# Kernel optimization log

Hardware: AMD Instinct MI355X
Metric: run time of the kernel (lower is better)

## Reference

```python
import jax, jax.numpy as jnp
import numpy as np

EMB = 2048
HEADS = 16
HEAD_DIM = EMB // HEADS
MIN_WINDOW = 64
MAX_WINDOW = 256
ROPE_BASE = 10000.0


def setup_inputs() -> dict:
    key = jax.random.key(0)
    ks = jax.random.split(key, 5)
    B, S = 2, 2048
    x = jax.random.normal(ks[0], (B, S, EMB), dtype=jnp.float32)
    w_qkv = jax.random.normal(ks[1], (3 * EMB, EMB), dtype=jnp.float32) * (EMB ** -0.5)
    w_out = jax.random.normal(ks[2], (EMB, EMB), dtype=jnp.float32) * (EMB ** -0.5)
    w_c1 = jax.random.normal(ks[3], (EMB // 4, EMB), dtype=jnp.float32) * 0.1 * (EMB ** -0.5)
    w_c2 = jax.random.normal(ks[4], (1, EMB // 4), dtype=jnp.float32) * 0.1 * ((EMB // 4) ** -0.5)
    return {"x": x, "w_qkv": w_qkv, "w_out": w_out, "w_c1": w_c1, "w_c2": w_c2}


def _rotate_half(t):
    # interleaved pairs: [-x1, x0, -x3, x2, ...]
    x1 = t[..., ::2]
    x2 = t[..., 1::2]
    return jnp.stack((-x2, x1), axis=-1).reshape(t.shape)


def _rope_tables(seq_len, dtype):
    inv_freq = 1.0 / (ROPE_BASE ** (jnp.arange(0, HEAD_DIM, 2, dtype=jnp.float32) / HEAD_DIM))
    pos = jnp.arange(seq_len, dtype=jnp.float32)
    freqs = jnp.outer(pos, inv_freq)                      # [S, D/2]
    emb = jnp.concatenate([freqs, freqs], axis=-1)        # [S, D]
    return jnp.cos(emb)[None, None].astype(dtype), jnp.sin(emb)[None, None].astype(dtype)


def _forward(x, w_qkv, w_out, w_c1, w_c2):
    B, S, _ = x.shape
    scale = HEAD_DIM ** -0.5

    qkv = x @ w_qkv.T                                     # [B, S, 3E]
    qkv = qkv.reshape(B, S, 3, HEADS, HEAD_DIM).transpose(2, 0, 3, 1, 4)
    q, k, v = qkv[0], qkv[1], qkv[2]                      # each [B, H, S, D]

    cos, sin = _rope_tables(S, x.dtype)
    q = q * cos + _rotate_half(q) * sin
    k = k * cos + _rotate_half(k) * sin

    scores = jnp.einsum("bhqd,bhkd->bhqk", q, k) * scale  # [B, H, S, S]

    # adaptive window size from input complexity
    var = jnp.var(x.reshape(B, -1), axis=1, ddof=1)        # torch unbiased var over dims [1,2]
    var_norm = jax.nn.sigmoid(var * 10.0 - 5.0)
    x_mean = x.mean(axis=1)                                # [B, E]
    hidden = jax.nn.silu(x_mean @ w_c1.T)
    learned = jax.nn.sigmoid(hidden @ w_c2.T)[:, 0]        # [B]
    complexity = (var_norm + learned) / 2.0
    window_f = MIN_WINDOW + complexity * (MAX_WINDOW - MIN_WINDOW)
    window = window_f.mean().astype(jnp.int32)             # trunc like .int()
    window = jnp.maximum(jnp.minimum(window, S), MIN_WINDOW)

    # causal + sliding-window mask: keep 0 <= q_pos - k_pos < window
    pos = jnp.arange(S)
    rel = pos[:, None] - pos[None, :]                      # [S, S]
    keep = (rel >= 0) & (rel < window)
    scores = jnp.where(keep[None, None], scores, -jnp.inf)

    attn = jax.nn.softmax(scores, axis=-1)
    out = jnp.einsum("bhqk,bhkd->bhqd", attn, v)           # [B, H, S, D]
    out = out.transpose(0, 2, 1, 3).reshape(B, S, EMB)
    return out @ w_out.T


def reference(x, w_qkv, w_out, w_c1, w_c2):
    return _forward(x, w_qkv, w_out, w_c1, w_c2)
```

## Files before the change

kernel.cpp:

```cpp
#include <hip/hip_runtime.h>
#include <math.h>


#define S_LEN 2048
#define EMB 2048
#define HEADS 16
#define HDIM 128
#define NT 20
#define PSTR 336

typedef _Float16 f16x8 __attribute__((ext_vector_type(8)));
typedef _Float16 f16x4 __attribute__((ext_vector_type(4)));
typedef float f32x4 __attribute__((ext_vector_type(4)));

__device__ __forceinline__ void gld16(const void* g, void* l) {
    __builtin_amdgcn_global_load_lds(
        (const __attribute__((address_space(1))) unsigned int*)g,
        (__attribute__((address_space(3))) unsigned int*)l, 16, 0, 0);
}

__global__ void rope_table(float2* __restrict__ cstab) {
    int s = blockIdx.x;
    int d = threadIdx.x;
    int j = d & 63;
    double inv = pow(10000.0, -(double)j / 64.0);
    double ang = (double)s * inv;
    cstab[s * HDIM + d] = make_float2((float)cos(ang), (float)sin(ang));
}

__global__ __launch_bounds__(256) void col_reduce(const float* __restrict__ x,
                                                  float* __restrict__ xmean_acc,
                                                  double* __restrict__ scal,
                                                  _Float16* __restrict__ x16) {
    int b = blockIdx.z;
    int cg = blockIdx.x;
    int sg = blockIdx.y;
    int e4 = cg * 256 + threadIdx.x;
    const size_t base = ((size_t)b * S_LEN + sg * 32) * EMB;
    const float4* xb = (const float4*)(x + base) + e4;
    f16x4* xo = (f16x4*)(x16 + base) + e4;
    double cs0 = 0.0, cs1 = 0.0, cs2 = 0.0, cs3 = 0.0;
    double cq = 0.0;
    for (int s = 0; s < 32; ++s) {
        float4 v = xb[(size_t)s * (EMB / 4)];
        f16x4 o;
        o.x = (_Float16)v.x; o.y = (_Float16)v.y;
        o.z = (_Float16)v.z; o.w = (_Float16)v.w;
        xo[(size_t)s * (EMB / 4)] = o;
        cs0 += v.x; cs1 += v.y; cs2 += v.z; cs3 += v.w;
        cq += (double)v.x * v.x + (double)v.y * v.y +
              (double)v.z * v.z + (double)v.w * v.w;
    }
    float* xm = xmean_acc + b * EMB + e4 * 4;
    atomicAdd(xm + 0, (float)cs0);
    atomicAdd(xm + 1, (float)cs1);
    atomicAdd(xm + 2, (float)cs2);
    atomicAdd(xm + 3, (float)cs3);
    __shared__ double rs[256], rq[256];
    rs[threadIdx.x] = cs0 + cs1 + cs2 + cs3;
    rq[threadIdx.x] = cq;
    __syncthreads();
    for (int off = 128; off > 0; off >>= 1) {
        if (threadIdx.x < off) {
            rs[threadIdx.x] += rs[threadIdx.x + off];
            rq[threadIdx.x] += rq[threadIdx.x + off];
        }
        __syncthreads();
    }
    if (threadIdx.x == 0) {
        atomicAdd(&scal[b], rs[0]);
        atomicAdd(&scal[2 + b], rq[0]);
    }
}

__global__ __launch_bounds__(256) void hidden_kernel(const float* __restrict__ xmean_acc,
                                                     const float* __restrict__ wc1,
                                                     float* __restrict__ hidden) {
    int j = blockIdx.x;
    int b = blockIdx.y;
    const float* xm = xmean_acc + b * EMB;
    const float* wr = wc1 + (size_t)j * EMB;
    double acc = 0.0;
    for (int k = threadIdx.x; k < EMB; k += 256)
        acc += (double)xm[k] * (double)wr[k];
    __shared__ double red[256];
    red[threadIdx.x] = acc;
    __syncthreads();
    for (int off = 128; off > 0; off >>= 1) {
        if (threadIdx.x < off) red[threadIdx.x] += red[threadIdx.x + off];
        __syncthreads();
    }
    if (threadIdx.x == 0) {
        double z = red[0] * (1.0 / 2048.0);
        hidden[b * 512 + j] = (float)(z / (1.0 + exp(-z)));
    }
}

__global__ __launch_bounds__(512) void window_kernel(const float* __restrict__ hidden,
                                                     const float* __restrict__ wc2,
                                                     const double* __restrict__ scal,
                                                     int* __restrict__ wout) {
    __shared__ double red[512];
    __shared__ double wfs[2];
    for (int b = 0; b < 2; ++b) {
        red[threadIdx.x] = (double)hidden[b * 512 + threadIdx.x] * (double)wc2[threadIdx.x];
        __syncthreads();
        for (int off = 256; off > 0; off >>= 1) {
            if (threadIdx.x < off) red[threadIdx.x] += red[threadIdx.x + off];
            __syncthreads();
        }
        if (threadIdx.x == 0) {
            double pre = red[0];
            double learned = 1.0 / (1.0 + exp(-pre));
            const double N = (double)S_LEN * (double)EMB;
            double sum = scal[b], sq = scal[2 + b];
            double var = (sq - sum * sum / N) / (N - 1.0);
            double vn = 1.0 / (1.0 + exp(-(var * 10.0 - 5.0)));
            double comp = 0.5 * (vn + learned);
            wfs[b] = 64.0 + comp * 192.0;
        }
        __syncthreads();
    }
    if (threadIdx.x == 0) {
        float wf = (float)(0.5 * (wfs[0] + wfs[1]));
        int w = (int)wf;
        if (w > S_LEN) w = S_LEN;
        if (w < 64) w = 64;
        *wout = w;
    }
}

#define NQKV4 3145728
#define NOUT4 1048576
__global__ __launch_bounds__(256) void cvt_weights(const float* __restrict__ wqkv,
                                                   const float* __restrict__ wout,
                                                   _Float16* __restrict__ d_qkv,
                                                   _Float16* __restrict__ d_out) {
    int i = blockIdx.x * 256 + threadIdx.x;
    const float4* s;
    f16x4* d;
    if (i < NQKV4) {
        s = (const float4*)wqkv + i;
        d = (f16x4*)d_qkv + i;
    } else {
        s = (const float4*)wout + (i - NQKV4);
        d = (f16x4*)d_out + (i - NQKV4);
    }
    float4 v = *s;
    f16x4 o;
    o.x = (_Float16)v.x; o.y = (_Float16)v.y;
    o.z = (_Float16)v.z; o.w = (_Float16)v.w;
    *d = o;
}

#define GEMM_PROLOGUE(An, Wn)                                                   \
    __shared__ _Float16 As[128 * 64];                                           \
    __shared__ _Float16 Bs[128 * 64];                                           \
    const int tid = threadIdx.x;                                                \
    const int lane = tid & 63;                                                  \
    const int wv = tid >> 6;                                                    \
    const int wm = wv >> 1, wn = wv & 1;                                        \
    const int m0 = blockIdx.y * 128;                                            \
    const int n0 = blockIdx.x * 128;                                            \
    const int lrow = lane >> 3;                                       \
    const int lchk = (lane & 7) ^ lrow;                       \
    const int srow = wv * 32 + lrow;                                            \
    const _Float16* agp = An + (size_t)(m0 + srow) * EMB + lchk * 8;            \
    const _Float16* bgp = Wn + (size_t)(n0 + srow) * EMB + lchk * 8;            \
    _Float16* al = &As[wv * 32 * 64];                                           \
    _Float16* bl = &Bs[wv * 32 * 64];                                           \
    const int frow = lane & 15;                                                 \
    const int fgrp = lane >> 4;                                                 \
    f32x4 acc[4][4] = {};                                                       \
    for (int k0 = 0; k0 < EMB; k0 += 64) {                                      \
        __syncthreads();                                                        \
        _Pragma("unroll")                                                       \
        for (int t = 0; t < 4; ++t) {                                           \
            gld16(agp + (size_t)t * 8 * EMB, al + t * 8 * 64);                  \
            gld16(bgp + (size_t)t * 8 * EMB, bl + t * 8 * 64);                  \
        }                                                                       \
        agp += 64; bgp += 64;                                                   \
        __syncthreads();                                                        \
        _Pragma("unroll")                                                       \
        for (int ks = 0; ks < 2; ++ks) {                                        \
            f16x8 af[4], bf[4];                                                 \
            _Pragma("unroll")                                                   \
            for (int i = 0; i < 4; ++i)                                         \
                af[i] = *(const f16x8*)&As[(wm * 64 + i * 16 + frow) * 64 +     \
                                           (((ks * 4 + fgrp) ^ (frow & 7)) * 8)]; \
            _Pragma("unroll")                                                   \
            for (int j = 0; j < 4; ++j)                                         \
                bf[j] = *(const f16x8*)&Bs[(wn * 64 + j * 16 + frow) * 64 +     \
                                           (((ks * 4 + fgrp) ^ (frow & 7)) * 8)]; \
            _Pragma("unroll")                                                   \
            for (int i = 0; i < 4; ++i)                                         \
                _Pragma("unroll")                                               \
                for (int j = 0; j < 4; ++j)                                     \
                    acc[i][j] = __builtin_amdgcn_mfma_f32_16x16x32_f16(         \
                        af[i], bf[j], acc[i][j], 0, 0, 0);                      \
        }                                                                       \
    }                                                                           \
    const int colbase = lane & 15;                                              \
    const int rowoff = (lane >> 4) * 4;

__global__ __launch_bounds__(256) void gemm_qkv_f16(const _Float16* __restrict__ An,
                                                    const _Float16* __restrict__ Wn,
                                                    _Float16* __restrict__ q16,
                                                    _Float16* __restrict__ k16,
                                                    _Float16* __restrict__ vt,
                                                    const float2* __restrict__ cstab) {
    GEMM_PROLOGUE(An, Wn)
    const int which = n0 >> 11;
    const int h = (n0 >> 7) & 15;
    if (which == 2) {
#pragma unroll
        for (int i = 0; i < 4; ++i) {
#pragma unroll
            for (int j = 0; j < 4; ++j) {
                const int d = wn * 64 + j * 16 + colbase;
                int m = m0 + wm * 64 + i * 16 + rowoff;
                int b = m >> 11, s = m & 2047;
                f16x4 o;
#pragma unroll
                for (int r = 0; r < 4; ++r) o[r] = (_Float16)acc[i][j][r];
                *(f16x4*)&vt[(((size_t)b * HEADS + h) * HDIM + d) * S_LEN + s] = o;
            }
        }
    } else {
        _Float16* dst = which == 0 ? q16 : k16;
        const float sgn = (colbase & 1) ? 1.f : -1.f;
#pragma unroll
        for (int i = 0; i < 4; ++i) {
#pragma unroll
            for (int j = 0; j < 4; ++j) {
                const int d = wn * 64 + j * 16 + colbase;
#pragma unroll
                for (int r = 0; r < 4; ++r) {
                    int m = m0 + wm * 64 + i * 16 + rowoff + r;
                    int b = m >> 11, s = m & 2047;
                    float a = acc[i][j][r];
                    float p = __shfl_xor(a, 1, 64);
                    float2 cs = cstab[(size_t)s * HDIM + d];
                    float o = fmaf(a, cs.x, sgn * p * cs.y);
                    dst[(((size_t)b * HEADS + h) * S_LEN + s) * HDIM + d] = (_Float16)o;
                }
            }
        }
    }
}

__global__ __launch_bounds__(256) void gemm_out_f16(const _Float16* __restrict__ An,
                                                    const _Float16* __restrict__ Wn,
                                                    float* __restrict__ C) {
    GEMM_PROLOGUE(An, Wn)
#pragma unroll
    for (int i = 0; i < 4; ++i) {
#pragma unroll
        for (int j = 0; j < 4; ++j) {
            const int n = n0 + wn * 64 + j * 16 + colbase;
#pragma unroll
            for (int r = 0; r < 4; ++r) {
                int m = m0 + wm * 64 + i * 16 + rowoff + r;
                C[(size_t)m * EMB + n] = acc[i][j][r];
            }
        }
    }
}

__global__ __launch_bounds__(256) void attn_mfma(const _Float16* __restrict__ q16,
                                                 const _Float16* __restrict__ k16,
                                                 const _Float16* __restrict__ v16t,
                                                 _Float16* __restrict__ ob,
                                                 const int* __restrict__ wptr) {
    const int q0 = blockIdx.x * 64;
    const int h = blockIdx.y;
    const int b = blockIdx.z;
    const int tid = threadIdx.x;
    const int lane = tid & 63;
    const int wv = tid >> 6;
    const int w = *wptr;

    __shared__ _Float16 Pl[4][16 * PSTR];
    _Float16* Pw = Pl[wv];

    const int kstart = q0 - 256;
    int ntlo_w = (257 - w) >> 4;
    int ntlo_n = q0 < 256 ? ((256 - q0) >> 4) : 0;
    const int ntlo = ntlo_w > ntlo_n ? ntlo_w : ntlo_n;

    const int frow = lane & 15;
    const int fgrp = lane >> 4;
    const int fcol = fgrp * 8;

    const size_t bh = (size_t)b * HEADS + h;
    const _Float16* Qp = q16 + (bh * S_LEN + q0 + wv * 16 + frow) * HDIM + fcol;
    const _Float16* Kb = k16 + bh * S_LEN * HDIM;
    const _Float16* Vt = v16t + bh * HDIM * S_LEN;

    f16x8 aq[4];
#pragma unroll
    for (int ks = 0; ks < 4; ++ks) aq[ks] = *(const f16x8*)(Qp + ks * 32);

    f32x4 accs[NT];
#pragma unroll
    for (int nt = 0; nt < NT; ++nt) accs[nt] = (f32x4){0.f, 0.f, 0.f, 0.f};
#pragma unroll
    for (int nt = 0; nt < NT; ++nt) {
        if (nt < ntlo) continue;
        int krow = kstart + nt * 16 + frow;
        if (krow < 0) krow = 0;
        const _Float16* kp = Kb + (size_t)krow * HDIM + fcol;
#pragma unroll
        for (int ks = 0; ks < 4; ++ks) {
            f16x8 bk = *(const f16x8*)(kp + ks * 32);
            accs[nt] = __builtin_amdgcn_mfma_f32_16x16x32_f16(aq[ks], bk, accs[nt], 0, 0, 0);
        }
    }

    const int qrow = fgrp * 4;
    const int qabs = q0 + wv * 16 + qrow;
    const float scale = 0.08838834764831845f;
    float mx[4] = {-INFINITY, -INFINITY, -INFINITY, -INFINITY};
#pragma unroll
    for (int nt = 0; nt < NT; ++nt) {
        int key = kstart + nt * 16 + frow;
#pragma unroll
        for (int r = 0; r < 4; ++r) {
            int rel = (qabs + r) - key;
            bool keep = (key >= 0) && (rel >= 0) && (rel < w);
            float s = keep ? accs[nt][r] * scale : -INFINITY;
            accs[nt][r] = s;
            mx[r] = fmaxf(mx[r], s);
        }
    }
#pragma unroll
    for (int r = 0; r < 4; ++r) {
        float m = mx[r];
#pragma unroll
        for (int off = 1; off < 16; off <<= 1)
            m = fmaxf(m, __shfl_xor(m, off, 64));
        mx[r] = m;
    }

    float ls[4] = {0.f, 0.f, 0.f, 0.f};
#pragma unroll
    for (int nt = 0; nt < NT; ++nt) {
#pragma unroll
        for (int r = 0; r < 4; ++r) {
            float p = __expf(accs[nt][r] - mx[r]);
            ls[r] += p;
            Pw[(qrow + r) * PSTR + nt * 16 + frow] = (_Float16)p;
        }
    }
    float inv[4];
#pragma unroll
    for (int r = 0; r < 4; ++r) {
        float l = ls[r];
#pragma unroll
        for (int off = 1; off < 16; off <<= 1)
            l += __shfl_xor(l, off, 64);
        inv[r] = 1.f / l;
    }

    const int pvlo = ntlo >> 1;
    f32x4 acco[8];
#pragma unroll
    for (int jt = 0; jt < 8; ++jt) acco[jt] = (f32x4){0.f, 0.f, 0.f, 0.f};
    const _Float16* Pr = &Pl[wv][frow * PSTR];
#pragma unroll
    for (int kp = 0; kp < 10; ++kp) {
        if (kp < pvlo) continue;
        f16x8 ap = *(const f16x8*)(Pr + kp * 32 + fcol);
        int kv = kstart + kp * 32 + fcol;
        if (kv < 0) kv = 0;
#pragma unroll
        for (int jt = 0; jt < 8; ++jt) {
            f16x8 bv = *(const f16x8*)(Vt + (size_t)(jt * 16 + frow) * S_LEN + kv);
            acco[jt] = __builtin_amdgcn_mfma_f32_16x16x32_f16(ap, bv, acco[jt], 0, 0, 0);
        }
    }

#pragma unroll
    for (int jt = 0; jt < 8; ++jt) {
#pragma unroll
        for (int r = 0; r < 4; ++r) {
            int s = qabs + r;
            ob[((size_t)b * S_LEN + s) * EMB + h * HDIM + jt * 16 + frow] =
                (_Float16)(acco[jt][r] * inv[r]);
        }
    }
}

extern "C" void kernel_launch(void* const* d_in, const int* in_sizes, int n_in,
                              void* d_out, int out_size, void* d_ws, size_t ws_size,
                              hipStream_t stream) {
    const float* x     = (const float*)d_in[0];
    const float* w_qkv = (const float*)d_in[1];
    const float* w_out = (const float*)d_in[2];
    const float* w_c1  = (const float*)d_in[3];
    const float* w_c2  = (const float*)d_in[4];
    float* out = (float*)d_out;
    char* ws = (char*)d_ws;

    double*    scal   = (double*)(ws + 0);
    int*       win    = (int*)(ws + 64);
    float*     xmean  = (float*)(ws + 128);
    float*     hidden = (float*)(ws + 16640);
    float2*    cstab  = (float2*)(ws + 32768);
    _Float16*  x16    = (_Float16*)(ws + 4194304);
    _Float16*  wqkv16 = (_Float16*)(ws + 20971520);
    _Float16*  ao16   = (_Float16*)(ws + 20971520);
    _Float16*  v16t   = (_Float16*)(ws + 46137344);
    _Float16*  q16    = (_Float16*)(ws + 62914560);
    _Float16*  k16    = (_Float16*)(ws + 79691776);
    _Float16*  wout16 = (_Float16*)(ws + 96468992);

    hipMemsetAsync(d_ws, 0, 32768, stream);

    rope_table<<<dim3(S_LEN), dim3(HDIM), 0, stream>>>(cstab);
    col_reduce<<<dim3(2, 64, 2), dim3(256), 0, stream>>>(x, xmean, scal, x16);
    hidden_kernel<<<dim3(512, 2), dim3(256), 0, stream>>>(xmean, w_c1, hidden);
    window_kernel<<<dim3(1), dim3(512), 0, stream>>>(hidden, w_c2, scal, win);

    cvt_weights<<<dim3((NQKV4 + NOUT4) / 256), dim3(256), 0, stream>>>(
        w_qkv, w_out, wqkv16, wout16);

    gemm_qkv_f16<<<dim3(48, 32), dim3(256), 0, stream>>>(x16, wqkv16, q16, k16, v16t, cstab);
    attn_mfma<<<dim3(32, HEADS, 2), dim3(256), 0, stream>>>(q16, k16, v16t, ao16, win);
    gemm_out_f16<<<dim3(16, 32), dim3(256), 0, stream>>>(ao16, wout16, out);
}
```

Baseline: 397.9 us.

## Use 256x128 double-buffered pipelined GEMM tiles with explicit waitcnt scheduling

Replaces the shared GEMM core with a 512-thread, 256x128-tile version. The K loop now uses double-buffered LDS split into two k-halves. Asynchronous global-to-LDS loads for later stages are issued while MFMAs run on the current stage, with explicit vmcnt waits, sched barriers and raised wave priority around the MFMA block. This targets the load/compute serialization of the old loop, which had two syncthreads per k-step, and improves operand reuse per block. In exchange it uses more LDS and registers per block, and the launch grids for both GEMMs shrink accordingly.

New measurement: 411.1 us. +3.3%, slower.

```diff
diff --git a/kernel.cpp b/kernel.cpp
--- a/kernel.cpp
+++ b/kernel.cpp
@@ -153,63 +153,97 @@
     *d = o;
 }
 
-#define GEMM_PROLOGUE(An, Wn)                                                   \
-    __shared__ _Float16 As[128 * 64];                                           \
-    __shared__ _Float16 Bs[128 * 64];                                           \
-    const int tid = threadIdx.x;                                                \
-    const int lane = tid & 63;                                                  \
-    const int wv = tid >> 6;                                                    \
-    const int wm = wv >> 1, wn = wv & 1;                                        \
-    const int m0 = blockIdx.y * 128;                                            \
-    const int n0 = blockIdx.x * 128;                                            \
-    const int lrow = lane >> 3;                                       \
-    const int lchk = (lane & 7) ^ lrow;                       \
-    const int srow = wv * 32 + lrow;                                            \
-    const _Float16* agp = An + (size_t)(m0 + srow) * EMB + lchk * 8;            \
-    const _Float16* bgp = Wn + (size_t)(n0 + srow) * EMB + lchk * 8;            \
-    _Float16* al = &As[wv * 32 * 64];                                           \
-    _Float16* bl = &Bs[wv * 32 * 64];                                           \
-    const int frow = lane & 15;                                                 \
-    const int fgrp = lane >> 4;                                                 \
-    f32x4 acc[4][4] = {};                                                       \
-    for (int k0 = 0; k0 < EMB; k0 += 64) {                                      \
-        __syncthreads();                                                        \
-        _Pragma("unroll")                                                       \
-        for (int t = 0; t < 4; ++t) {                                           \
-            gld16(agp + (size_t)t * 8 * EMB, al + t * 8 * 64);                  \
-            gld16(bgp + (size_t)t * 8 * EMB, bl + t * 8 * 64);                  \
-        }                                                                       \
-        agp += 64; bgp += 64;                                                   \
-        __syncthreads();                                                        \
-        _Pragma("unroll")                                                       \
-        for (int ks = 0; ks < 2; ++ks) {                                        \
-            f16x8 af[4], bf[4];                                                 \
-            _Pragma("unroll")                                                   \
-            for (int i = 0; i < 4; ++i)                                         \
-                af[i] = *(const f16x8*)&As[(wm * 64 + i * 16 + frow) * 64 +     \
-                                           (((ks * 4 + fgrp) ^ (frow & 7)) * 8)]; \
-            _Pragma("unroll")                                                   \
-            for (int j = 0; j < 4; ++j)                                         \
-                bf[j] = *(const f16x8*)&Bs[(wn * 64 + j * 16 + frow) * 64 +     \
-                                           (((ks * 4 + fgrp) ^ (frow & 7)) * 8)]; \
-            _Pragma("unroll")                                                   \
-            for (int i = 0; i < 4; ++i)                                         \
-                _Pragma("unroll")                                               \
-                for (int j = 0; j < 4; ++j)                                     \
-                    acc[i][j] = __builtin_amdgcn_mfma_f32_16x16x32_f16(         \
-                        af[i], bf[j], acc[i][j], 0, 0, 0);                      \
-        }                                                                       \
-    }                                                                           \
-    const int colbase = lane & 15;                                              \
+#define NKT 32
+
+#define STAGE(bufc, khc, koff)                                              \
+    gld16(aS0 + (koff), &As[bufc][khc][wv * 512]);                          \
+    gld16(aS1 + (koff), &As[bufc][khc][(8 + wv) * 512]);                    \
+    gld16(bS + (koff), &Bs[bufc][khc][wv * 512]);
+
+#define VM6 asm volatile("s_waitcnt vmcnt(6)" ::: "memory");
+#define VM3 asm volatile("s_waitcnt vmcnt(3)" ::: "memory");
+#define VM0 asm volatile("s_waitcnt vmcnt(0)" ::: "memory");
+#define VMX
+
+#define PHASE(bufc, ksc, VM, ...)                                           \
+    {                                                                       \
+        f16x8 af[4], bf[4];                                                 \
+        _Pragma("unroll")                                                   \
+        for (int i_ = 0; i_ < 4; ++i_)                                      \
+            af[i_] = *(const f16x8*)&As[bufc][ksc][aoff + i_ * 512];        \
+        _Pragma("unroll")                                                   \
+        for (int j_ = 0; j_ < 4; ++j_)                                      \
+            bf[j_] = *(const f16x8*)&Bs[bufc][ksc][boff + j_ * 512];        \
+        __VA_ARGS__                                                         \
+        __builtin_amdgcn_sched_barrier(0);                                  \
+        __builtin_amdgcn_s_barrier();                                       \
+        asm volatile("s_waitcnt lgkmcnt(0)" ::: "memory");                  \
+        __builtin_amdgcn_sched_barrier(0);                                  \
+        __builtin_amdgcn_s_setprio(1);                                      \
+        _Pragma("unroll")                                                   \
+        for (int i_ = 0; i_ < 4; ++i_)                                      \
+            _Pragma("unroll")                                               \
+            for (int j_ = 0; j_ < 4; ++j_)                                  \
+                acc[i_][j_] = __builtin_amdgcn_mfma_f32_16x16x32_f16(       \
+                    af[i_], bf[j_], acc[i_][j_], 0, 0, 0);                  \
+        __builtin_amdgcn_s_setprio(0);                                      \
+        __builtin_amdgcn_sched_barrier(0);                                  \
+        VM                                                                  \
+        __builtin_amdgcn_s_barrier();                                       \
+        __builtin_amdgcn_sched_barrier(0);                                  \
+    }
+
+#define GEMM256_CORE(An, Wn)                                                \
+    __shared__ __align__(16) _Float16 As[2][2][8192];                       \
+    __shared__ __align__(16) _Float16 Bs[2][2][4096];                       \
+    const int tid = threadIdx.x;                                            \
+    const int lane = tid & 63;                                              \
+    const int wv = tid >> 6;                                                \
+    const int wm = wv >> 1, wn = wv & 1;                                    \
+    const int m0 = blockIdx.y * 256;                                        \
+    const int n0 = blockIdx.x * 128;                                        \
+                          \
+    const int g = (lane & 7) ^ (lane >> 3);                                 \
+    const int rb = 2 * (lane >> 3) + (g >> 2);                              \
+    const int kq = (g & 3) * 8;                                             \
+    const _Float16* aS0 = An + (size_t)(m0 + wv * 16 + rb) * EMB + kq;      \
+    const _Float16* aS1 = aS0 + (size_t)128 * EMB;                          \
+    const _Float16* bS = Wn + (size_t)(n0 + wv * 16 + rb) * EMB + kq;       \
+                      \
+    const int frow = lane & 15, fgrp = lane >> 4;                           \
+    const int srl = frow >> 1;                                              \
+    const int cst = (((frow & 1) << 2) + fgrp) ^ srl;                       \
+    const int aoff = (wm * 32 + srl) * 64 + cst * 8;                        \
+    const int boff = (wn * 32 + srl) * 64 + cst * 8;                        \
+    f32x4 acc[4][4] = {};                                                   \
+             \
+    STAGE(0, 0, 0)                                                          \
+    STAGE(0, 1, 32)                                                         \
+    STAGE(1, 0, 64)                                                         \
+    VM6                                                                     \
+    __builtin_amdgcn_s_barrier();                                           \
+    __builtin_amdgcn_sched_barrier(0);                                      \
+    for (int kt = 0; kt < NKT - 2; kt += 2) {                               \
+        const int kb = kt * 64;                                             \
+        PHASE(0, 0, VM6, STAGE(1, 1, kb + 96))                              \
+        PHASE(0, 1, VM6, STAGE(0, 0, kb + 128))                             \
+        PHASE(1, 0, VM6, STAGE(0, 1, kb + 160))                             \
+        PHASE(1, 1, VM6, STAGE(1, 0, kb + 192))                             \
+    }                                                                       \
+    PHASE(0, 0, VM6, STAGE(1, 1, 2016))                                     \
+    PHASE(0, 1, VM3)                                                        \
+    PHASE(1, 0, VM0)                                                        \
+    PHASE(1, 1, VMX)                                                        \
+    const int colbase = lane & 15;                                          \
     const int rowoff = (lane >> 4) * 4;
 
-__global__ __launch_bounds__(256) void gemm_qkv_f16(const _Float16* __restrict__ An,
-                                                    const _Float16* __restrict__ Wn,
-                                                    _Float16* __restrict__ q16,
-                                                    _Float16* __restrict__ k16,
-                                                    _Float16* __restrict__ vt,
-                                                    const float2* __restrict__ cstab) {
-    GEMM_PROLOGUE(An, Wn)
+__global__ __launch_bounds__(512, 2) void gemm_qkv_f16(const _Float16* __restrict__ An,
+                                                       const _Float16* __restrict__ Wn,
+                                                       _Float16* __restrict__ q16,
+                                                       _Float16* __restrict__ k16,
+                                                       _Float16* __restrict__ vt,
+                                                       const float2* __restrict__ cstab) {
+    GEMM256_CORE(An, Wn)
     const int which = n0 >> 11;
     const int h = (n0 >> 7) & 15;
     if (which == 2) {
@@ -249,10 +283,10 @@
     }
 }
 
-__global__ __launch_bounds__(256) void gemm_out_f16(const _Float16* __restrict__ An,
-                                                    const _Float16* __restrict__ Wn,
-                                                    float* __restrict__ C) {
-    GEMM_PROLOGUE(An, Wn)
+__global__ __launch_bounds__(512, 2) void gemm_out_f16(const _Float16* __restrict__ An,
+                                                       const _Float16* __restrict__ Wn,
+                                                       float* __restrict__ C) {
+    GEMM256_CORE(An, Wn)
 #pragma unroll
     for (int i = 0; i < 4; ++i) {
 #pragma unroll
@@ -425,7 +459,7 @@
     cvt_weights<<<dim3((NQKV4 + NOUT4) / 256), dim3(256), 0, stream>>>(
         w_qkv, w_out, wqkv16, wout16);
 
-    gemm_qkv_f16<<<dim3(48, 32), dim3(256), 0, stream>>>(x16, wqkv16, q16, k16, v16t, cstab);
+    gemm_qkv_f16<<<dim3(48, 16), dim3(512), 0, stream>>>(x16, wqkv16, q16, k16, v16t, cstab);
     attn_mfma<<<dim3(32, HEADS, 2), dim3(256), 0, stream>>>(q16, k16, v16t, ao16, win);
-    gemm_out_f16<<<dim3(16, 32), dim3(256), 0, stream>>>(ao16, wout16, out);
-}
+    gemm_out_f16<<<dim3(16, 16), dim3(512), 0, stream>>>(ao16, wout16, out);
+}
```
